# Optimization experiments

Hardware: AMD Instinct MI355X
Metric: run time of the kernel (lower is better)

Reference implementation:

```python
import jax, jax.numpy as jnp
import numpy as np

U = 256   # units
D = 256   # input_dim
B = 65536 # batch


def hard_tanh(x):
    return jnp.clip(x, -1.0, 1.0)


def binarize(x):
    # sign quantization (forward); straight-through in the bwd module
    return jnp.where(x >= 0, 1.0, -1.0).astype(x.dtype)


def setup_inputs() -> dict:
    key = jax.random.key(0)
    k1, k2, k3, k4, k5 = jax.random.split(key, 5)
    return {
        "inputs": jax.random.normal(k1, (B, D), dtype=jnp.float32),
        "h": jax.random.normal(k2, (B, U), dtype=jnp.float32),
        "c": jax.random.normal(k3, (B, U), dtype=jnp.float32),
        "kernel": jax.random.normal(k4, (D, 4 * U), dtype=jnp.float32) * 0.05,
        "recurrent_kernel": jax.random.normal(k5, (U, 4 * U), dtype=jnp.float32) * 0.05,
    }


def reference(inputs, h, c, kernel, recurrent_kernel):
    u = kernel.shape[1] // 4
    h_tm1 = hard_tanh(h)
    c_tm1 = hard_tanh(c)
    # binarized input projection, hard_tanh applied to each gate pre-activation
    x_all = hard_tanh(inputs @ binarize(kernel))            # [B, 4U]
    x_i, x_f, x_c, x_o = (x_all[:, :u], x_all[:, u:2*u],
                          x_all[:, 2*u:3*u], x_all[:, 3*u:])
    # binarized recurrent projection
    r_all = h_tm1 @ binarize(recurrent_kernel)              # [B, 4U]
    r_i, r_f, r_c, r_o = (r_all[:, :u], r_all[:, u:2*u],
                          r_all[:, 2*u:3*u], r_all[:, 3*u:])
    # NOTE: faithful to source: f pairs x_i with W_f, i pairs x_f with W_i
    f = hard_tanh(x_i + r_f)
    i = hard_tanh(x_f + r_i)
    c_new = f * c_tm1 + i * hard_tanh(x_c + r_c)
    o = hard_tanh(x_o + r_o)
    h_new = hard_tanh(o * hard_tanh(c_new))
    return (h_new, h_new, c_new)
```

## Files before the change

kernel.cpp:

```cpp
#include <hip/hip_runtime.h>


#define NB 65536

typedef _Float16 f16x8 __attribute__((ext_vector_type(8)));
typedef float f32x16 __attribute__((ext_vector_type(16)));

__device__ __forceinline__ float htanh(float x) { return fminf(1.f, fmaxf(-1.f, x)); }

__global__ void prep_w(const float* __restrict__ Kf, const float* __restrict__ RKf,
                       unsigned short* __restrict__ wfrag) {
  __shared__ unsigned short sgn[32][72];
  const int b = blockIdx.x;
  const int side = b >> 7, kt = (b >> 4) & 7, nt = b & 15;
  const float* M = side ? RKf : Kf;
  const int t = threadIdx.x;

  {
    const int k = t >> 3, n8 = (t & 7) << 3;
    const float* p = M + (kt * 32 + k) * 1024 + nt * 64 + n8;
    float4 v0 = *(const float4*)p;
    float4 v1 = *(const float4*)(p + 4);
    float xs[8] = {v0.x, v0.y, v0.z, v0.w, v1.x, v1.y, v1.z, v1.w};
#pragma unroll
    for (int i = 0; i < 8; ++i)
      sgn[k][n8 + i] = (xs[i] >= 0.f) ? 0x3C00u : 0xBC00u;
  }
  __syncthreads();

  const int fl = t >> 6, l = t & 63;
  const int j = fl >> 1, uh = fl & 1;
  const int nloc = uh * 32 + (l & 31);
  const int kloc = j * 16 + (l >> 5) * 8;
  unsigned short o[8];
#pragma unroll
  for (int e = 0; e < 8; ++e) o[e] = sgn[kloc + e][nloc];
  const int ng = nt * 64 + nloc;
  const int gate = ng >> 8, u32 = (ng >> 5) & 7;
  const int fragid = (((kt * 2 + j) * 2 + side) * 4 + gate) * 8 + u32;
  uint4 ov;
  ov.x = (unsigned)o[0] | ((unsigned)o[1] << 16);
  ov.y = (unsigned)o[2] | ((unsigned)o[3] << 16);
  ov.z = (unsigned)o[4] | ((unsigned)o[5] << 16);
  ov.w = (unsigned)o[6] | ((unsigned)o[7] << 16);
  *(uint4*)((char*)wfrag + fragid * 1024 + l * 16) = ov;
}

__global__ __launch_bounds__(256, 3)
void blstm_main(const float* __restrict__ xin, const float* __restrict__ hin,
                const float* __restrict__ cin, const unsigned short* __restrict__ wfrag,
                float* __restrict__ out) {
  __shared__ char smem[32768];

  const int bid = blockIdx.x;
  const int swz = (bid & 7) * 1024 + (bid >> 3);
  const int mb = swz >> 2, ub = swz & 3;
  const int m0 = mb << 5;
  const int u0 = ub << 6;

  const int tid = threadIdx.x;
  const int lane = tid & 63;
  const int w = tid >> 6;
  const int wu = w & 1, wg = w >> 1;
  const int l31 = lane & 31, lh = lane >> 5;

  const int sSide = tid >> 7;
  const int sRow = (tid & 127) >> 2;
  const int sQ = tid & 3;
  const float* aPtr = (sSide ? hin : xin) + (m0 + sRow) * 256 + (sQ << 3);
  char* const aWr = smem + sSide * 4096 + sRow * 128;
  const int swzHi = ((sQ ^ (sRow & 7)) << 4);
  const int swzLo = (((sQ + 4) ^ (sRow & 7)) << 4);

  const char* const wbase = (const char*)wfrag + lane * 16;

  f32x16 acc[4] = {};

  float4 a0 = *(const float4*)(aPtr);
  float4 a1 = *(const float4*)(aPtr + 4);

  for (int s = 0; s < 8; ++s) {
    {
      char* wr = aWr + (s & 1) * 8192;
      float xs[8] = {a0.x, a0.y, a0.z, a0.w, a1.x, a1.y, a1.z, a1.w};
      f16x8 hv, lv;
#pragma unroll
      for (int i = 0; i < 8; ++i) {
        float x = xs[i];
        if (sSide) x = htanh(x);
        _Float16 hf = (_Float16)x;
        hv[i] = hf;
        lv[i] = (_Float16)(x - (float)hf);
      }
      *(f16x8*)(wr + swzHi) = hv;
      *(f16x8*)(wr + swzLo) = lv;
    }

    f16x8 wfr[2][4];
#pragma unroll
    for (int j = 0; j < 2; ++j)
#pragma unroll
      for (int nf = 0; nf < 4; ++nf) {
        const int side = nf >> 1, gate = wg * 2 + (nf & 1);
        const int fragid = (((s * 2 + j) * 2 + side) * 4 + gate) * 8 + (ub * 2 + wu);
        wfr[j][nf] = *(const f16x8*)(wbase + fragid * 1024);
      }
    if (s < 7) {
      a0 = *(const float4*)(aPtr + (s + 1) * 32);
      a1 = *(const float4*)(aPtr + (s + 1) * 32 + 4);
    }

    __syncthreads();

    const char* rd = smem + (s & 1) * 8192;
#pragma unroll
    for (int j = 0; j < 2; ++j) {
#pragma unroll
      for (int hl = 0; hl < 2; ++hl) {
        f16x8 af[2];
#pragma unroll
        for (int side = 0; side < 2; ++side)
          af[side] = *(const f16x8*)(rd + side * 4096 + l31 * 128 +
                       ((((hl << 2) | (j << 1) | lh) ^ (l31 & 7)) << 4));
#pragma unroll
        for (int nf = 0; nf < 4; ++nf)
          acc[nf] = __builtin_amdgcn_mfma_f32_32x32x16_f16(af[nf >> 1], wfr[j][nf],
                                                           acc[nf], 0, 0, 0);
      }
    }
  }

  float* ex = (float*)(smem + 16384 + wu * 8192);

  if (wg == 1) {
    float4 c4[4], o4[4];
#pragma unroll
    for (int r = 0; r < 16; ++r) {
      float cand = htanh(htanh(acc[0][r]) + acc[2][r]);
      float og   = htanh(htanh(acc[1][r]) + acc[3][r]);
      ((float*)&c4[r >> 2])[r & 3] = cand;
      ((float*)&o4[r >> 2])[r & 3] = og;
    }
#pragma unroll
    for (int c = 0; c < 4; ++c) {
      *(float4*)((char*)ex + c * 1024 + lane * 16) = c4[c];
      *(float4*)((char*)ex + 4096 + c * 1024 + lane * 16) = o4[c];
    }
  }
  __syncthreads();
  if (wg == 0) {
    float4 c4[4], o4[4];
#pragma unroll
    for (int c = 0; c < 4; ++c) {
      c4[c] = *(const float4*)((const char*)ex + c * 1024 + lane * 16);
      o4[c] = *(const float4*)((const char*)ex + 4096 + c * 1024 + lane * 16);
    }
#pragma unroll
    for (int r = 0; r < 16; ++r) {
      const int row = (r & 3) + ((r >> 2) << 3) + (lh << 2);
      const int grow = m0 + row;
      const int gu = u0 + wu * 32 + l31;
      const float fg = htanh(htanh(acc[0][r]) + acc[3][r]);
      const float ig = htanh(htanh(acc[1][r]) + acc[2][r]);
      const float cand = ((const float*)&c4[r >> 2])[r & 3];
      const float og   = ((const float*)&o4[r >> 2])[r & 3];
      const float ct = htanh(cin[grow * 256 + gu]);
      const float cn = fg * ct + ig * cand;
      const float hn = htanh(og * htanh(cn));
      const int o1 = grow * 256 + gu;
      out[o1] = hn;
      out[NB * 256 + o1] = hn;
      out[2 * NB * 256 + o1] = cn;
    }
  }
}

extern "C" void kernel_launch(void* const* d_in, const int* in_sizes, int n_in,
                              void* d_out, int out_size, void* d_ws, size_t ws_size,
                              hipStream_t stream) {
  const float* xin = (const float*)d_in[0];
  const float* hin = (const float*)d_in[1];
  const float* cin = (const float*)d_in[2];
  const float* kf  = (const float*)d_in[3];
  const float* rkf = (const float*)d_in[4];
  float* out = (float*)d_out;

  unsigned short* wfrag = (unsigned short*)d_ws;

  prep_w<<<256, 256, 0, stream>>>(kf, rkf, wfrag);
  blstm_main<<<8192, 256, 0, stream>>>(xin, hin, cin, wfrag, out);
}
```

Before: 204.3 us.

## Reorder weight fragment layout and prefetch next-step weights during MFMA compute

The weight fragment layout is permuted so that the eight fragments a wave needs per k-step sit in a contiguous 4 KB region. The main loop is manually unrolled so the next step's weight fragments load after the current MFMAs are issued, rather than just before the barrier. The plain __syncthreads is replaced by an explicit lgkmcnt wait, raw s_barrier and sched_barrier, which removes the vmcnt wait that previously blocked on outstanding global loads. This is meant to hide global-load latency behind compute, at the cost of more live registers and possible occupancy pressure.

```diff
diff --git a/kernel.cpp b/kernel.cpp
--- a/kernel.cpp
+++ b/kernel.cpp
@@ -37,7 +37,7 @@
   for (int e = 0; e < 8; ++e) o[e] = sgn[kloc + e][nloc];
   const int ng = nt * 64 + nloc;
   const int gate = ng >> 8, u32 = (ng >> 5) & 7;
-  const int fragid = (((kt * 2 + j) * 2 + side) * 4 + gate) * 8 + u32;
+  const int fragid = (((kt * 2 + j) * 8 + u32) * 4 + gate) * 2 + side;
   uint4 ov;
   ov.x = (unsigned)o[0] | ((unsigned)o[1] << 16);
   ov.y = (unsigned)o[2] | ((unsigned)o[3] << 16);
@@ -72,63 +72,80 @@
   const int swzHi = ((sQ ^ (sRow & 7)) << 4);
   const int swzLo = (((sQ + 4) ^ (sRow & 7)) << 4);
 
-  const char* const wbase = (const char*)wfrag + lane * 16;
+  const char* const wq = (const char*)wfrag + ((ub * 2 + wu) << 13) + (wg << 12) + lane * 16;
 
   f32x16 acc[4] = {};
-
-  float4 a0 = *(const float4*)(aPtr);
-  float4 a1 = *(const float4*)(aPtr + 4);
-
-  for (int s = 0; s < 8; ++s) {
-    {
-      char* wr = aWr + (s & 1) * 8192;
-      float xs[8] = {a0.x, a0.y, a0.z, a0.w, a1.x, a1.y, a1.z, a1.w};
-      f16x8 hv, lv;
-#pragma unroll
-      for (int i = 0; i < 8; ++i) {
-        float x = xs[i];
-        if (sSide) x = htanh(x);
-        _Float16 hf = (_Float16)x;
-        hv[i] = hf;
-        lv[i] = (_Float16)(x - (float)hf);
-      }
-      *(f16x8*)(wr + swzHi) = hv;
-      *(f16x8*)(wr + swzLo) = lv;
-    }
-
-    f16x8 wfr[2][4];
-#pragma unroll
-    for (int j = 0; j < 2; ++j)
-#pragma unroll
-      for (int nf = 0; nf < 4; ++nf) {
-        const int side = nf >> 1, gate = wg * 2 + (nf & 1);
-        const int fragid = (((s * 2 + j) * 2 + side) * 4 + gate) * 8 + (ub * 2 + wu);
-        wfr[j][nf] = *(const f16x8*)(wbase + fragid * 1024);
-      }
-    if (s < 7) {
-      a0 = *(const float4*)(aPtr + (s + 1) * 32);
-      a1 = *(const float4*)(aPtr + (s + 1) * 32 + 4);
-    }
-
-    __syncthreads();
-
-    const char* rd = smem + (s & 1) * 8192;
-#pragma unroll
-    for (int j = 0; j < 2; ++j) {
-#pragma unroll
-      for (int hl = 0; hl < 2; ++hl) {
-        f16x8 af[2];
-#pragma unroll
-        for (int side = 0; side < 2; ++side)
-          af[side] = *(const f16x8*)(rd + side * 4096 + l31 * 128 +
-                       ((((hl << 2) | (j << 1) | lh) ^ (l31 & 7)) << 4));
-#pragma unroll
-        for (int nf = 0; nf < 4; ++nf)
-          acc[nf] = __builtin_amdgcn_mfma_f32_32x32x16_f16(af[nf >> 1], wfr[j][nf],
-                                                           acc[nf], 0, 0, 0);
-      }
-    }
-  }
+  f16x8 wfr[2][4];
+  float4 a0, a1;
+
+  a0 = *(const float4*)(aPtr);
+  a1 = *(const float4*)(aPtr + 4);
+#define WLOAD(S) do {                                                     \
+    const char* p0_ = wq + (S) * 2 * 65536;                               \
+    const char* p1_ = wq + ((S) * 2 + 1) * 65536;                         \
+    wfr[0][0] = *(const f16x8*)(p0_);                                     \
+    wfr[0][1] = *(const f16x8*)(p0_ + 2048);                              \
+    wfr[0][2] = *(const f16x8*)(p0_ + 1024);                              \
+    wfr[0][3] = *(const f16x8*)(p0_ + 3072);                              \
+    wfr[1][0] = *(const f16x8*)(p1_);                                     \
+    wfr[1][1] = *(const f16x8*)(p1_ + 2048);                              \
+    wfr[1][2] = *(const f16x8*)(p1_ + 1024);                              \
+    wfr[1][3] = *(const f16x8*)(p1_ + 3072);                              \
+  } while (0)
+  WLOAD(0);
+
+#define STEP(S) do {                                                      \
+      \
+    float4 c0_ = a0, c1_ = a1;                                            \
+    if ((S) < 7) {                                                        \
+      a0 = *(const float4*)(aPtr + ((S) + 1) * 32);                       \
+      a1 = *(const float4*)(aPtr + ((S) + 1) * 32 + 4);                   \
+    }                                                                     \
+    {                                                                     \
+      char* wr_ = aWr + ((S) & 1) * 8192;                                 \
+      float xs_[8] = {c0_.x, c0_.y, c0_.z, c0_.w, c1_.x, c1_.y, c1_.z, c1_.w}; \
+      f16x8 hv_, lv_;                                                     \
+      _Pragma("unroll")                                                   \
+      for (int i_ = 0; i_ < 8; ++i_) {                                    \
+        float x_ = xs_[i_];                                               \
+        if (sSide) x_ = htanh(x_);                                        \
+        _Float16 hf_ = (_Float16)x_;                                      \
+        hv_[i_] = hf_;                                                    \
+        lv_[i_] = (_Float16)(x_ - (float)hf_);                            \
+      }                                                                   \
+      *(f16x8*)(wr_ + swzHi) = hv_;                                       \
+      *(f16x8*)(wr_ + swzLo) = lv_;                                       \
+    }                                                                     \
+    asm volatile("s_waitcnt lgkmcnt(0)" ::: "memory");                    \
+    __builtin_amdgcn_s_barrier();                                         \
+    __builtin_amdgcn_sched_barrier(0);                                    \
+    asm volatile("" ::: "memory");                                        \
+    {                                                                     \
+      const char* rd_ = smem + ((S) & 1) * 8192;                          \
+      _Pragma("unroll")                                                   \
+      for (int j_ = 0; j_ < 2; ++j_) {                                    \
+        _Pragma("unroll")                                                 \
+        for (int hl_ = 0; hl_ < 2; ++hl_) {                               \
+          f16x8 af_[2];                                                   \
+          _Pragma("unroll")                                               \
+          for (int sd_ = 0; sd_ < 2; ++sd_)                               \
+            af_[sd_] = *(const f16x8*)(rd_ + sd_ * 4096 + l31 * 128 +     \
+                         ((((hl_ << 2) | (j_ << 1) | lh) ^ (l31 & 7)) << 4)); \
+          _Pragma("unroll")                                               \
+          for (int nf_ = 0; nf_ < 4; ++nf_)                               \
+            acc[nf_] = __builtin_amdgcn_mfma_f32_32x32x16_f16(            \
+                af_[nf_ >> 1], wfr[j_][nf_], acc[nf_], 0, 0, 0);          \
+        }                                                                 \
+      }                                                                   \
+    }                                                                     \
+     \
+    if ((S) < 7) WLOAD((S) + 1);                                          \
+  } while (0)
+
+  STEP(0); STEP(1); STEP(2); STEP(3);
+  STEP(4); STEP(5); STEP(6); STEP(7);
+#undef STEP
+#undef WLOAD
 
   float* ex = (float*)(smem + 16384 + wu * 8192);
 
```

New measurement: 204.2 us. About the same (-0.0%).

## Split waves by input/recurrent side and restructure weight fragment layout and LDS staging

Applied to the files above, without the earlier changes.

Reassigns waves so each wave pair handles one side (input or recurrent projection) across all four gates, changing the weight fragment ordering so each wave's four fragments are contiguous. It replaces the XOR-swizzled A tile with a padded LDS layout, hand-unrolls the k-loop with split weight loads interleaved around the MFMAs, and uses a raw waitcnt+barrier. The epilogue now exchanges full recurrent accumulators through LDS rather than partially reduced gates. Launch bounds rise to 4 blocks per SM to raise occupancy, which may pressure registers.

```diff
diff --git a/kernel.cpp b/kernel.cpp
--- a/kernel.cpp
+++ b/kernel.cpp
@@ -29,15 +29,16 @@
   __syncthreads();
 
   const int fl = t >> 6, l = t & 63;
-  const int j = fl >> 1, uh = fl & 1;
-  const int nloc = uh * 32 + (l & 31);
+  const int j = fl >> 1, uhh = fl & 1;
+  const int nloc = uhh * 32 + (l & 31);
   const int kloc = j * 16 + (l >> 5) * 8;
   unsigned short o[8];
 #pragma unroll
   for (int e = 0; e < 8; ++e) o[e] = sgn[kloc + e][nloc];
   const int ng = nt * 64 + nloc;
   const int gate = ng >> 8, u32 = (ng >> 5) & 7;
-  const int fragid = (((kt * 2 + j) * 2 + side) * 4 + gate) * 8 + u32;
+  const int k16 = kt * 2 + j;
+  const int fragid = ((k16 * 2 + side) * 8 + u32) * 4 + gate;
   uint4 ov;
   ov.x = (unsigned)o[0] | ((unsigned)o[1] << 16);
   ov.y = (unsigned)o[2] | ((unsigned)o[3] << 16);
@@ -46,7 +47,7 @@
   *(uint4*)((char*)wfrag + fragid * 1024 + l * 16) = ov;
 }
 
-__global__ __launch_bounds__(256, 3)
+__global__ __launch_bounds__(256, 4)
 void blstm_main(const float* __restrict__ xin, const float* __restrict__ hin,
                 const float* __restrict__ cin, const unsigned short* __restrict__ wfrag,
                 float* __restrict__ out) {
@@ -54,123 +55,139 @@
 
   const int bid = blockIdx.x;
   const int swz = (bid & 7) * 1024 + (bid >> 3);
-  const int mb = swz >> 2, ub = swz & 3;
-  const int m0 = mb << 5;
-  const int u0 = ub << 6;
+  const int m0 = (swz >> 2) << 5;
+  const int ub = swz & 3;
 
   const int tid = threadIdx.x;
   const int lane = tid & 63;
   const int w = tid >> 6;
-  const int wu = w & 1, wg = w >> 1;
+  const int wu = w & 1, sw = w >> 1;
   const int l31 = lane & 31, lh = lane >> 5;
 
   const int sSide = tid >> 7;
   const int sRow = (tid & 127) >> 2;
   const int sQ = tid & 3;
-  const float* aPtr = (sSide ? hin : xin) + (m0 + sRow) * 256 + (sQ << 3);
-  char* const aWr = smem + sSide * 4096 + sRow * 128;
-  const int swzHi = ((sQ ^ (sRow & 7)) << 4);
-  const int swzLo = (((sQ + 4) ^ (sRow & 7)) << 4);
-
-  const char* const wbase = (const char*)wfrag + lane * 16;
+  const float* aPtr = (sSide ? hin : xin) + (m0 + sRow) * 256 + sQ * 8;
+  char* const aWr = smem + sSide * 4224 + sQ * 528 + sRow * 16;
+  const char* const aRd = smem + sw * 4224 + lh * 528 + l31 * 16;
+
+  const unsigned short* const wq = wfrag + ((sw * 8 + ub * 2 + wu) << 11) + lane * 8;
 
   f32x16 acc[4] = {};
-
+  f16x8 wf[4];
+  f16x8 ah, al;
   float4 a0 = *(const float4*)(aPtr);
   float4 a1 = *(const float4*)(aPtr + 4);
 
-  for (int s = 0; s < 8; ++s) {
-    {
-      char* wr = aWr + (s & 1) * 8192;
-      float xs[8] = {a0.x, a0.y, a0.z, a0.w, a1.x, a1.y, a1.z, a1.w};
-      f16x8 hv, lv;
-#pragma unroll
-      for (int i = 0; i < 8; ++i) {
-        float x = xs[i];
-        if (sSide) x = htanh(x);
-        _Float16 hf = (_Float16)x;
-        hv[i] = hf;
-        lv[i] = (_Float16)(x - (float)hf);
+#define MFMA4(AF) do {                                                      \
+    acc[0] = __builtin_amdgcn_mfma_f32_32x32x16_f16(AF, wf[0], acc[0], 0, 0, 0); \
+    acc[1] = __builtin_amdgcn_mfma_f32_32x32x16_f16(AF, wf[1], acc[1], 0, 0, 0); \
+    acc[2] = __builtin_amdgcn_mfma_f32_32x32x16_f16(AF, wf[2], acc[2], 0, 0, 0); \
+    acc[3] = __builtin_amdgcn_mfma_f32_32x32x16_f16(AF, wf[3], acc[3], 0, 0, 0); \
+  } while (0)
+
+#define STEP(S) do {                                                        \
+          \
+    {                                                                       \
+      float xs_[8] = {a0.x, a0.y, a0.z, a0.w, a1.x, a1.y, a1.z, a1.w};      \
+      f16x8 hv_, lv_;                                                       \
+      _Pragma("unroll")                                                     \
+      for (int i_ = 0; i_ < 8; ++i_) {                                      \
+        float x_ = xs_[i_];                                                 \
+        if (sSide) x_ = htanh(x_);                                          \
+        _Float16 hf_ = (_Float16)x_;                                        \
+        hv_[i_] = hf_;                                                      \
+        lv_[i_] = (_Float16)(x_ - (float)hf_);                              \
+      }                                                                     \
+      char* wr_ = aWr + ((S) & 1) * 8448;                                   \
+      *(f16x8*)(wr_) = hv_;                                                 \
+      *(f16x8*)(wr_ + 2112) = lv_;                                          \
+    }                                                                       \
+    if ((S) < 7) {                                                          \
+      a0 = *(const float4*)(aPtr + ((S) + 1) * 32);                         \
+      a1 = *(const float4*)(aPtr + ((S) + 1) * 32 + 4);                     \
+    }                                                                       \
+                 \
+    {                                                                       \
+      const unsigned short* wp_ = wq + ((S) * 2) * 32768;                   \
+      wf[0] = *(const f16x8*)(wp_);                                         \
+      wf[1] = *(const f16x8*)(wp_ + 512);                                   \
+      wf[2] = *(const f16x8*)(wp_ + 1024);                                  \
+      wf[3] = *(const f16x8*)(wp_ + 1536);                                  \
+    }                                                                       \
+    asm volatile("s_waitcnt lgkmcnt(0)\n\ts_barrier" ::: "memory");         \
+    {                                                                       \
+      const char* rd_ = aRd + ((S) & 1) * 8448;                             \
+      ah = *(const f16x8*)(rd_);                                \
+      al = *(const f16x8*)(rd_ + 2112);                         \
+      MFMA4(ah);                                                            \
+      MFMA4(al);                                                            \
+                 \
+      const unsigned short* wp_ = wq + ((S) * 2 + 1) * 32768;               \
+      wf[0] = *(const f16x8*)(wp_);                                         \
+      wf[1] = *(const f16x8*)(wp_ + 512);                                   \
+      wf[2] = *(const f16x8*)(wp_ + 1024);                                  \
+      wf[3] = *(const f16x8*)(wp_ + 1536);                                  \
+      ah = *(const f16x8*)(rd_ + 1056);                         \
+      al = *(const f16x8*)(rd_ + 2112 + 1056);                  \
+      MFMA4(ah);                                                            \
+      MFMA4(al);                                                            \
+    }                                                                       \
+  } while (0)
+
+  STEP(0); STEP(1); STEP(2); STEP(3);
+  STEP(4); STEP(5); STEP(6); STEP(7);
+#undef STEP
+#undef MFMA4
+
+  __syncthreads();
+  float* ex = (float*)(smem + wu * 16384);
+
+  if (sw == 1) {
+#pragma unroll
+    for (int g = 0; g < 4; ++g)
+#pragma unroll
+      for (int q = 0; q < 4; ++q) {
+        float4 v;
+        v.x = acc[g][q * 4 + 0]; v.y = acc[g][q * 4 + 1];
+        v.z = acc[g][q * 4 + 2]; v.w = acc[g][q * 4 + 3];
+        *(float4*)((char*)ex + (g * 4 + q) * 1024 + lane * 16) = v;
       }
-      *(f16x8*)(wr + swzHi) = hv;
-      *(f16x8*)(wr + swzLo) = lv;
-    }
-
-    f16x8 wfr[2][4];
-#pragma unroll
-    for (int j = 0; j < 2; ++j)
-#pragma unroll
-      for (int nf = 0; nf < 4; ++nf) {
-        const int side = nf >> 1, gate = wg * 2 + (nf & 1);
-        const int fragid = (((s * 2 + j) * 2 + side) * 4 + gate) * 8 + (ub * 2 + wu);
-        wfr[j][nf] = *(const f16x8*)(wbase + fragid * 1024);
-      }
-    if (s < 7) {
-      a0 = *(const float4*)(aPtr + (s + 1) * 32);
-      a1 = *(const float4*)(aPtr + (s + 1) * 32 + 4);
-    }
-
-    __syncthreads();
-
-    const char* rd = smem + (s & 1) * 8192;
-#pragma unroll
-    for (int j = 0; j < 2; ++j) {
-#pragma unroll
-      for (int hl = 0; hl < 2; ++hl) {
-        f16x8 af[2];
-#pragma unroll
-        for (int side = 0; side < 2; ++side)
-          af[side] = *(const f16x8*)(rd + side * 4096 + l31 * 128 +
-                       ((((hl << 2) | (j << 1) | lh) ^ (l31 & 7)) << 4));
-#pragma unroll
-        for (int nf = 0; nf < 4; ++nf)
-          acc[nf] = __builtin_amdgcn_mfma_f32_32x32x16_f16(af[nf >> 1], wfr[j][nf],
-                                                           acc[nf], 0, 0, 0);
-      }
-    }
-  }
-
-  float* ex = (float*)(smem + 16384 + wu * 8192);
-
-  if (wg == 1) {
-    float4 c4[4], o4[4];
-#pragma unroll
-    for (int r = 0; r < 16; ++r) {
-      float cand = htanh(htanh(acc[0][r]) + acc[2][r]);
-      float og   = htanh(htanh(acc[1][r]) + acc[3][r]);
-      ((float*)&c4[r >> 2])[r & 3] = cand;
-      ((float*)&o4[r >> 2])[r & 3] = og;
-    }
-#pragma unroll
-    for (int c = 0; c < 4; ++c) {
-      *(float4*)((char*)ex + c * 1024 + lane * 16) = c4[c];
-      *(float4*)((char*)ex + 4096 + c * 1024 + lane * 16) = o4[c];
-    }
   }
   __syncthreads();
-  if (wg == 0) {
-    float4 c4[4], o4[4];
-#pragma unroll
-    for (int c = 0; c < 4; ++c) {
-      c4[c] = *(const float4*)((const char*)ex + c * 1024 + lane * 16);
-      o4[c] = *(const float4*)((const char*)ex + 4096 + c * 1024 + lane * 16);
-    }
-#pragma unroll
-    for (int r = 0; r < 16; ++r) {
-      const int row = (r & 3) + ((r >> 2) << 3) + (lh << 2);
-      const int grow = m0 + row;
-      const int gu = u0 + wu * 32 + l31;
-      const float fg = htanh(htanh(acc[0][r]) + acc[3][r]);
-      const float ig = htanh(htanh(acc[1][r]) + acc[2][r]);
-      const float cand = ((const float*)&c4[r >> 2])[r & 3];
-      const float og   = ((const float*)&o4[r >> 2])[r & 3];
-      const float ct = htanh(cin[grow * 256 + gu]);
-      const float cn = fg * ct + ig * cand;
-      const float hn = htanh(og * htanh(cn));
-      const int o1 = grow * 256 + gu;
-      out[o1] = hn;
-      out[NB * 256 + o1] = hn;
-      out[2 * NB * 256 + o1] = cn;
+  if (sw == 0) {
+    const int gu = ub * 64 + wu * 32 + l31;
+#pragma unroll
+    for (int q = 0; q < 4; ++q) {
+      float4 ri = *(const float4*)((const char*)ex + (0 * 4 + q) * 1024 + lane * 16);
+      float4 rf = *(const float4*)((const char*)ex + (1 * 4 + q) * 1024 + lane * 16);
+      float4 rc = *(const float4*)((const char*)ex + (2 * 4 + q) * 1024 + lane * 16);
+      float4 ro = *(const float4*)((const char*)ex + (3 * 4 + q) * 1024 + lane * 16);
+#pragma unroll
+      for (int t = 0; t < 4; ++t) {
+        const int r = q * 4 + t;
+        const int row = t + q * 8 + lh * 4;
+        const int grow = m0 + row;
+        const float xi = htanh(acc[0][r]);
+        const float xf = htanh(acc[1][r]);
+        const float xc = htanh(acc[2][r]);
+        const float xo = htanh(acc[3][r]);
+        const float riv = ((const float*)&ri)[t];
+        const float rfv = ((const float*)&rf)[t];
+        const float rcv = ((const float*)&rc)[t];
+        const float rov = ((const float*)&ro)[t];
+        const float fg   = htanh(xi + rfv);
+        const float ig   = htanh(xf + riv);
+        const float cand = htanh(xc + rcv);
+        const float og   = htanh(xo + rov);
+        const float ct = htanh(cin[grow * 256 + gu]);
+        const float cn = fg * ct + ig * cand;
+        const float hn = htanh(og * htanh(cn));
+        const int o1 = grow * 256 + gu;
+        out[o1] = hn;
+        out[NB * 256 + o1] = hn;
+        out[2 * NB * 256 + o1] = cn;
+      }
     }
   }
 }
```

Result: faster. 199.2 us (-2.5%).
